# Kernel tuning notes

Hardware: AMD Instinct MI355X
Metric: run time of the kernel (lower is better)

## Reference

```python
import jax, jax.numpy as jnp
import numpy as np

N, M, D = 131072, 128, 128

def setup_inputs() -> dict:
    key = jax.random.key(0)
    k1, k2, k3 = jax.random.split(key, 3)
    X = jax.random.normal(k1, (N, D), dtype=jnp.float32)
    r = jax.random.uniform(k2, (N, M), dtype=jnp.float32)
    mus = jax.random.normal(k3, (M, D), dtype=jnp.float32)
    return {"X": X, "r": r, "mus": mus}

def reference(X, r, mus):
    # Squared pairwise L2 distances without materializing [N, M, D]:
    x2 = jnp.sum(X * X, axis=1)            # [N]
    mu2 = jnp.sum(mus * mus, axis=1)       # [M]
    cross = X @ mus.T                      # [N, M]
    dist2 = jnp.maximum(x2[:, None] + mu2[None, :] - 2.0 * cross, 0.0)
    loss = jnp.sum(r * dist2) / X.shape[0]
    return loss
```

## Files before the change

kernel.cpp:

```cpp
#include <hip/hip_runtime.h>
#include <hip/hip_bf16.h>


typedef __attribute__((ext_vector_type(8)))  short  short8;
typedef __attribute__((ext_vector_type(16))) float  float16v;

#if defined(__has_builtin)
#if __has_builtin(__builtin_amdgcn_cvt_pk_bf16_f32)
#define HAVE_PK_BF16 1
#endif
#endif

__device__ __forceinline__ unsigned int pk_bf16(float x, float y) {
#ifdef HAVE_PK_BF16
    typedef __attribute__((ext_vector_type(2))) __bf16 bf16x2;
    bf16x2 p = __builtin_amdgcn_cvt_pk_bf16_f32(x, y);
    return __builtin_bit_cast(unsigned int, p);
#else
    unsigned int ux = __float_as_uint(x);
    unsigned int uy = __float_as_uint(y);
    ux += 0x7fffu + ((ux >> 16) & 1u);
    uy += 0x7fffu + ((uy >> 16) & 1u);
    return (ux >> 16) | (uy & 0xffff0000u);
#endif
}

__global__ void zero_ws_kernel(float* ws) { ws[threadIdx.x] = 0.0f; }

__global__ void final_reduce_kernel(const float* ws, float* out) {
    const int lane = threadIdx.x;
    float t = ws[lane];
    #pragma unroll
    for (int off = 32; off > 0; off >>= 1) t += __shfl_down(t, off);
    if (lane == 0) out[0] = t * (1.0f / 131072.0f);
}

__global__ __launch_bounds__(256, 3)
void isoloss_kernel(const float* __restrict__ X,
                    const float* __restrict__ r,
                    const float* __restrict__ mus,
                    float* __restrict__ ws)
{
    const int tid  = threadIdx.x;
    const int wave = tid >> 6;
    const int lane = tid & 63;
    const int col  = lane & 31;
    const int half = lane >> 5;

    __shared__ float wsum[4];

    short8 bfrag[8];
    float mu2p = 0.0f;
    {
        const float* mrow = mus + (size_t)(wave * 32 + col) * 128 + half * 8;
        #pragma unroll
        for (int ks = 0; ks < 8; ++ks) {
            const float4 a = *(const float4*)(mrow + ks * 16);
            const float4 b = *(const float4*)(mrow + ks * 16 + 4);
            mu2p += a.x*a.x + a.y*a.y + a.z*a.z + a.w*a.w
                  + b.x*b.x + b.y*b.y + b.z*b.z + b.w*b.w;
            union { short8 s8; uint4 u4; } u;
            u.u4.x = pk_bf16(a.x, a.y);
            u.u4.y = pk_bf16(a.z, a.w);
            u.u4.z = pk_bf16(b.x, b.y);
            u.u4.w = pk_bf16(b.z, b.w);
            bfrag[ks] = u.s8;
        }
    }
    const float mu2 = mu2p + __shfl_xor(mu2p, 32);
    float4 mu2q[4];
    #pragma unroll
    for (int q = 0; q < 4; ++q) {
        mu2q[q].x = __shfl(mu2, q * 8 + half * 4 + 0);
        mu2q[q].y = __shfl(mu2, q * 8 + half * 4 + 1);
        mu2q[q].z = __shfl(mu2, q * 8 + half * 4 + 2);
        mu2q[q].w = __shfl(mu2, q * 8 + half * 4 + 3);
    }

    float s = 0.0f;

    for (int g = blockIdx.x; g < 4096; g += gridDim.x) {
        const int rowbase = g * 32;
        const float* xp = X + (size_t)(rowbase + col) * 128 + half * 8;
        const float* rp = r + (size_t)(rowbase + col) * 128 + wave * 32 + half * 4;

        float4 xa[8], xb[8];
        #pragma unroll
        for (int ks = 0; ks < 8; ++ks) {
            xa[ks] = *(const float4*)(xp + ks * 16);
            xb[ks] = *(const float4*)(xp + ks * 16 + 4);
        }
        float4 rv[4];
        #pragma unroll
        for (int q = 0; q < 4; ++q)
            rv[q] = *(const float4*)(rp + q * 8);

        __builtin_amdgcn_sched_barrier(0);

        float16v acc = {};
        float p = 0.0f;
        #pragma unroll
        for (int ks = 0; ks < 8; ++ks) {
            const float4 a = xa[ks];
            const float4 b = xb[ks];
            p += a.x*a.x + a.y*a.y + a.z*a.z + a.w*a.w
               + b.x*b.x + b.y*b.y + b.z*b.z + b.w*b.w;
            union { short8 s8; uint4 u4; } u;
            u.u4.x = pk_bf16(a.x, a.y);
            u.u4.y = pk_bf16(a.z, a.w);
            u.u4.z = pk_bf16(b.x, b.y);
            u.u4.w = pk_bf16(b.z, b.w);
            acc = __builtin_amdgcn_mfma_f32_32x32x16_bf16(bfrag[ks], u.s8, acc, 0, 0, 0);
        }
        const float x2v = p + __shfl_xor(p, 32);

        #pragma unroll
        for (int q = 0; q < 4; ++q) {
            const float4 rq = rv[q];
            const float4 m2 = mu2q[q];
            s += rq.x * fmaxf(x2v + m2.x - 2.0f * acc[q * 4 + 0], 0.0f);
            s += rq.y * fmaxf(x2v + m2.y - 2.0f * acc[q * 4 + 1], 0.0f);
            s += rq.z * fmaxf(x2v + m2.z - 2.0f * acc[q * 4 + 2], 0.0f);
            s += rq.w * fmaxf(x2v + m2.w - 2.0f * acc[q * 4 + 3], 0.0f);
        }
    }

    #pragma unroll
    for (int off = 32; off > 0; off >>= 1) s += __shfl_down(s, off);
    if (lane == 0) wsum[wave] = s;
    __syncthreads();
    if (tid == 0)
        atomicAdd(&ws[blockIdx.x & 63], wsum[0] + wsum[1] + wsum[2] + wsum[3]);
}

extern "C" void kernel_launch(void* const* d_in, const int* in_sizes, int n_in,
                              void* d_out, int out_size, void* d_ws, size_t ws_size,
                              hipStream_t stream) {
    const float* X   = (const float*)d_in[0];
    const float* r   = (const float*)d_in[1];
    const float* mus = (const float*)d_in[2];
    float* out = (float*)d_out;
    float* ws  = (float*)d_ws;

    zero_ws_kernel<<<1, 64, 0, stream>>>(ws);
    isoloss_kernel<<<1024, 256, 0, stream>>>(X, r, mus, ws);
    final_reduce_kernel<<<1, 64, 0, stream>>>(ws, out);
}
```

Before: 164.6 us.

## Double-buffer X and r tiles in LDS via async global_load_lds DMA

Replaces direct per-thread global loads of X and r with asynchronous global-to-LDS copies into two LDS buffers, prefetching the next 32-row tile while the current one is computed. Uses an XOR swizzle on the LDS layout to avoid bank conflicts, and hardcodes a grid of 512 blocks each doing exactly 8 tiles. Occupancy drops to 2 blocks per CU because of the 64KB of LDS, and correctness now depends on the fixed grid size and the manual waitcnt encodings.

Measured after the change: 151.5 us. 8.0% less time.

```diff
diff --git a/kernel.cpp b/kernel.cpp
--- a/kernel.cpp
+++ b/kernel.cpp
@@ -25,6 +25,21 @@
 #endif
 }
 
+#define AS1 __attribute__((address_space(1)))
+#define AS3 __attribute__((address_space(3)))
+
+__device__ __forceinline__ void dma16(const void* g, void* l) {
+    __builtin_amdgcn_global_load_lds((const AS1 void*)g, (AS3 void*)l, 16, 0, 0);
+}
+
+__device__ __forceinline__ void wait_vm8() { __builtin_amdgcn_s_waitcnt(0x0F78); }
+__device__ __forceinline__ void wait_vm0() { __builtin_amdgcn_s_waitcnt(0x0F70); }
+__device__ __forceinline__ void barrier_nodrain() {
+    asm volatile("" ::: "memory");
+    __builtin_amdgcn_s_barrier();
+    asm volatile("" ::: "memory");
+}
+
 __global__ void zero_ws_kernel(float* ws) { ws[threadIdx.x] = 0.0f; }
 
 __global__ void final_reduce_kernel(const float* ws, float* out) {
@@ -35,7 +50,7 @@
     if (lane == 0) out[0] = t * (1.0f / 131072.0f);
 }
 
-__global__ __launch_bounds__(256, 3)
+__global__ __launch_bounds__(256, 2)
 void isoloss_kernel(const float* __restrict__ X,
                     const float* __restrict__ r,
                     const float* __restrict__ mus,
@@ -47,6 +62,10 @@
     const int col  = lane & 31;
     const int half = lane >> 5;
 
+    __shared__ __align__(16) unsigned char ldsX0[16384];
+    __shared__ __align__(16) unsigned char ldsX1[16384];
+    __shared__ __align__(16) unsigned char ldsR0[16384];
+    __shared__ __align__(16) unsigned char ldsR1[16384];
     __shared__ float wsum[4];
 
     short8 bfrag[8];
@@ -77,52 +96,82 @@
         mu2q[q].w = __shfl(mu2, q * 8 + half * 4 + 3);
     }
 
+    int goff[4];
+    #pragma unroll
+    for (int t = 0; t < 4; ++t) {
+        const int p   = (wave * 4 + t) * 64 + lane;
+        const int row = p >> 5;
+        goff[t] = row * 512 + (((lane & 31) ^ row) << 4);
+    }
+
+    const int   g0 = blockIdx.x;
+    const char* Xc = (const char*)X;
+    const char* Rc = (const char*)r;
+
+    {
+        const char* xg = Xc + (size_t)g0 * 16384;
+        const char* rg = Rc + (size_t)g0 * 16384;
+        #pragma unroll
+        for (int t = 0; t < 4; ++t) {
+            dma16(xg + goff[t], ldsX0 + (wave * 4 + t) * 1024);
+            dma16(rg + goff[t], ldsR0 + (wave * 4 + t) * 1024);
+        }
+    }
+
     float s = 0.0f;
 
-    for (int g = blockIdx.x; g < 4096; g += gridDim.x) {
-        const int rowbase = g * 32;
-        const float* xp = X + (size_t)(rowbase + col) * 128 + half * 8;
-        const float* rp = r + (size_t)(rowbase + col) * 128 + wave * 32 + half * 4;
+    #pragma unroll
+    for (int i = 0; i < 8; ++i) {
+        unsigned char* bx  = (i & 1) ? ldsX1 : ldsX0;
+        unsigned char* br  = (i & 1) ? ldsR1 : ldsR0;
+        unsigned char* bxn = (i & 1) ? ldsX0 : ldsX1;
+        unsigned char* brn = (i & 1) ? ldsR0 : ldsR1;
 
-        float4 xa[8], xb[8];
-        #pragma unroll
-        for (int ks = 0; ks < 8; ++ks) {
-            xa[ks] = *(const float4*)(xp + ks * 16);
-            xb[ks] = *(const float4*)(xp + ks * 16 + 4);
+        if (i < 7) {
+            const int gn = g0 + (i + 1) * 512;
+            const char* xg = Xc + (size_t)gn * 16384;
+            const char* rg = Rc + (size_t)gn * 16384;
+            #pragma unroll
+            for (int t = 0; t < 4; ++t) {
+                dma16(xg + goff[t], bxn + (wave * 4 + t) * 1024);
+                dma16(rg + goff[t], brn + (wave * 4 + t) * 1024);
+            }
+            wait_vm8();
+        } else {
+            wait_vm0();
         }
-        float4 rv[4];
-        #pragma unroll
-        for (int q = 0; q < 4; ++q)
-            rv[q] = *(const float4*)(rp + q * 8);
-
-        __builtin_amdgcn_sched_barrier(0);
+        barrier_nodrain();
 
         float16v acc = {};
         float p = 0.0f;
         #pragma unroll
         for (int ks = 0; ks < 8; ++ks) {
-            const float4 a = xa[ks];
-            const float4 b = xb[ks];
-            p += a.x*a.x + a.y*a.y + a.z*a.z + a.w*a.w
-               + b.x*b.x + b.y*b.y + b.z*b.z + b.w*b.w;
+            const int cc = ks * 4 + half * 2;
+            const float4 f0 = *(const float4*)(bx + col * 512 + (((cc    ) ^ col) << 4));
+            const float4 f1 = *(const float4*)(bx + col * 512 + (((cc + 1) ^ col) << 4));
+            p += f0.x*f0.x + f0.y*f0.y + f0.z*f0.z + f0.w*f0.w
+               + f1.x*f1.x + f1.y*f1.y + f1.z*f1.z + f1.w*f1.w;
             union { short8 s8; uint4 u4; } u;
-            u.u4.x = pk_bf16(a.x, a.y);
-            u.u4.y = pk_bf16(a.z, a.w);
-            u.u4.z = pk_bf16(b.x, b.y);
-            u.u4.w = pk_bf16(b.z, b.w);
+            u.u4.x = pk_bf16(f0.x, f0.y);
+            u.u4.y = pk_bf16(f0.z, f0.w);
+            u.u4.z = pk_bf16(f1.x, f1.y);
+            u.u4.w = pk_bf16(f1.z, f1.w);
             acc = __builtin_amdgcn_mfma_f32_32x32x16_bf16(bfrag[ks], u.s8, acc, 0, 0, 0);
         }
         const float x2v = p + __shfl_xor(p, 32);
 
         #pragma unroll
         for (int q = 0; q < 4; ++q) {
-            const float4 rq = rv[q];
+            const int cq = (wave * 8 + half + q * 2) ^ col;
+            const float4 rq = *(const float4*)(br + col * 512 + (cq << 4));
             const float4 m2 = mu2q[q];
             s += rq.x * fmaxf(x2v + m2.x - 2.0f * acc[q * 4 + 0], 0.0f);
             s += rq.y * fmaxf(x2v + m2.y - 2.0f * acc[q * 4 + 1], 0.0f);
             s += rq.z * fmaxf(x2v + m2.z - 2.0f * acc[q * 4 + 2], 0.0f);
             s += rq.w * fmaxf(x2v + m2.w - 2.0f * acc[q * 4 + 3], 0.0f);
         }
+
+        if (i < 7) barrier_nodrain();
     }
 
     #pragma unroll
@@ -143,6 +192,6 @@
     float* ws  = (float*)d_ws;
 
     zero_ws_kernel<<<1, 64, 0, stream>>>(ws);
-    isoloss_kernel<<<1024, 256, 0, stream>>>(X, r, mus, ws);
+    isoloss_kernel<<<512, 256, 0, stream>>>(X, r, mus, ws);
     final_reduce_kernel<<<1, 64, 0, stream>>>(ws, out);
 }
```
